# Performance work log

Hardware: AMD Instinct MI355X
Metric: run time of the kernel (lower is better)

## Reference

```python
import jax, jax.numpy as jnp
import numpy as np

N, IN_DIM, HID, OUT, NH = 512, 256, 256, 256, 4
HD = OUT // NH  # head_dim = 64
EPS = 1e-5


def _mlp(x, w1, b1, w2, b2):
    return jax.nn.relu(x @ w1 + b1) @ w2 + b2


def setup_inputs() -> dict:
    key = jax.random.key(0)
    ks = jax.random.split(key, 32)

    def rn(k, shape, fan_in):
        return (jax.random.normal(k, shape, jnp.float32) / np.float32(np.sqrt(fan_in)))

    V = jax.random.normal(ks[0], (N, IN_DIM), jnp.float32)
    adj = jax.random.randint(ks[1], (N, N), 0, 2, jnp.int32)
    adj = adj.at[jnp.arange(N), jnp.arange(N)].set(1)  # self-edges: avoid all -inf rows
    prev_hidden = jax.random.normal(ks[2], (N, HID), jnp.float32)
    z = jnp.zeros
    return dict(
        V=V, adj=adj, prev_hidden=prev_hidden,
        W1=rn(ks[3], (IN_DIM, HID), IN_DIM),
        a_std0=rn(ks[4], (HID, 1), HID), a_std1=rn(ks[5], (HID, 1), HID),
        ce_w1=rn(ks[6], (2 * IN_DIM, HID), 2 * IN_DIM), ce_b1=z((HID,), jnp.float32),
        ce_w2=rn(ks[7], (HID, HD), HID), ce_b2=z((HD,), jnp.float32),
        a_c0=rn(ks[8], (HD, 1), HD), a_c1=rn(ks[9], (HD, 1), HD),
        te_w1=rn(ks[10], (IN_DIM + HID, HID), IN_DIM + HID), te_b1=z((HID,), jnp.float32),
        te_w2=rn(ks[11], (HID, HD), HID), te_b2=z((HD,), jnp.float32),
        a_t0=rn(ks[12], (HD, 1), HD), a_t1=rn(ks[13], (HD, 1), HD),
        co_w1=rn(ks[14], (3 * IN_DIM, HID), 3 * IN_DIM), co_b1=z((HID,), jnp.float32),
        co_w2=rn(ks[15], (HID, HD), HID), co_b2=z((HD,), jnp.float32),
        a_co0=rn(ks[16], (HD, 1), HD), a_co1=rn(ks[17], (HD, 1), HD),
        W2=rn(ks[18], (HID + 2 * HD + 1, OUT), HID + 2 * HD + 1),
        Wo=rn(ks[19], (OUT, OUT), OUT), bo=z((OUT,), jnp.float32),
        ln_g=jnp.ones((OUT,), jnp.float32), ln_b=z((OUT,), jnp.float32),
    )


def reference(V, adj, prev_hidden, W1, a_std0, a_std1,
              ce_w1, ce_b1, ce_w2, ce_b2, a_c0, a_c1,
              te_w1, te_b1, te_w2, te_b2, a_t0, a_t1,
              co_w1, co_b1, co_w2, co_b2, a_co0, a_co1,
              W2, Wo, bo, ln_g, ln_b):
    ninf = -jnp.inf

    # ---- standard GAT branch -> H1: (N, HID) ----
    Wh1 = V @ W1
    s1 = Wh1 @ a_std0 + (Wh1 @ a_std1).T                      # (N, N)
    s1 = jnp.where(adj == 0, ninf, s1)
    H1 = jax.nn.softmax(s1, axis=1) @ Wh1

    # ---- causal branch: all ordered pairs i!=j, global softmax -> H2: (N, HD) ----
    pair = jnp.concatenate([jnp.broadcast_to(V[:, None, :], (N, N, IN_DIM)),
                            jnp.broadcast_to(V[None, :, :], (N, N, IN_DIM))], axis=-1)
    cf = _mlp(pair, ce_w1, ce_b1, ce_w2, ce_b2)               # (N, N, HD)
    cs = (cf @ (a_c0 + a_c1))[..., 0]                         # (N, N)
    cs = jnp.where(jnp.eye(N, dtype=bool), ninf, cs)          # exclude i==j pairs
    ca = jax.nn.softmax(cs.reshape(-1)).reshape(N, N, 1)
    H2 = jnp.broadcast_to((ca * cf).sum((0, 1)), (N, HD))

    # ---- temporal branch: (N,1) scores broadcast against causal mask -> running mean ----
    tf = _mlp(jnp.concatenate([V, prev_hidden], axis=-1), te_w1, te_b1, te_w2, te_b2)  # (N, HD)
    ts = tf @ (a_t0 + a_t1)                                   # (N, 1)
    cmask = jnp.triu(jnp.ones((N, N), bool), 1)
    tsb = jnp.where(cmask, ninf, jnp.broadcast_to(ts, (N, N)))
    H3 = jax.nn.softmax(tsb, axis=1) @ tf                     # (N, HD)

    # ---- coop branch: first two neighbors by index; size-1 softmax; buggy pad -> (N,1) ----
    order = jnp.argsort((1 - adj).astype(jnp.int32), axis=1, stable=True)  # adj==1 first, index order
    nb = V[order[:, :2]]                                      # (N, 2, IN_DIM)
    valid = ((adj == 1).sum(axis=1) >= 2)
    nb = jnp.where(valid[:, None, None], nb, jnp.zeros_like(nb))
    ci = jnp.concatenate([V, nb[:, 0], nb[:, 1]], axis=-1)    # (N, 3*IN_DIM)
    cf4 = _mlp(ci, co_w1, co_b1, co_w2, co_b2)                # (N, HD)
    ca4 = jax.nn.softmax(cf4 @ (a_co0 + a_co1), axis=1)       # (N,1): softmax over size-1 -> ones
    h4vec = (ca4.T @ cf4)[0]                                  # (HD,)
    # original: squeeze(-2)->(HD,), dim==1 -> unsqueeze(-1)->(HD,1), zero-pad rows to N
    H4 = jnp.zeros((N, 1), V.dtype).at[:HD, 0].set(h4vec)

    # ---- combine, lazy W2, proj, LN, ELU (dropout identity in eval) ----
    Hc = jnp.concatenate([H1, H2, H3, H4], axis=-1) @ W2      # (N, OUT)
    out = Hc @ Wo + bo
    mu = out.mean(-1, keepdims=True)
    var = ((out - mu) ** 2).mean(-1, keepdims=True)
    out = (out - mu) / jnp.sqrt(var + EPS) * ln_g + ln_b
    return jax.nn.elu(out)
```

## Files before the change

### kernel.cpp

```cpp
#include <hip/hip_runtime.h>
#include <math.h>

#define NN 512
#define HD 64
#define EPSV 1e-5f

struct GD {
  const float *A, *A2, *A3, *A4;
  const int* I;
  const float *B, *bias;
  float* C;
  int M, K, Nn, mode, act;
};

#define GEMM_SMEM (8704 + 17408 + 2176)
#define MEGA_SMEM 38656

__device__ __forceinline__ void gemm_body(char* smem, const GD& d, int bx, int by) {
  float (*At)[34] = (float (*)[34])smem;
  float (*Bs)[68] = (float (*)[68])(smem + 8704);
  char* extra = smem + 8704 + 17408;
  int* nbl = (int*)extra;
  float* wscl = (float*)extra;
  float* rowsuml = wscl + 512;

  const int t = threadIdx.x;
  const int tx = t & 15, ty = t >> 4;
  const int rowbase = by * 32, colbase = bx * 64;
  const int K = d.K, Nn = d.Nn, mode = d.mode, M = d.M;
  if (rowbase >= M) return;

  if (mode == 2) {
    int wave = t >> 6, lane = t & 63;
    for (int rr = wave; rr < 32; rr += 4) {
      int row = rowbase + rr;
      int n0 = -1, n1 = -1, cnt = 0;
      for (int c = 0; c < 8; ++c) {
        unsigned long long mm = __ballot(d.I[row * NN + c * 64 + lane] != 0);
        cnt += (int)__popcll(mm);
        if (n0 < 0 && mm) { n0 = c * 64 + (int)__builtin_ctzll(mm); mm &= mm - 1; }
        if (n1 < 0 && mm) { n1 = c * 64 + (int)__builtin_ctzll(mm); }
      }
      if (lane == 0) { nbl[rr * 3] = n0; nbl[rr * 3 + 1] = n1; nbl[rr * 3 + 2] = (cnt >= 2); }
    }
    __syncthreads();
  } else if (mode == 4) {
    wscl[t] = d.A2[t];
    wscl[256 + t] = d.A2[256 + t];
    __syncthreads();
  }

  float4 aR[2], bR[4];
  float rs0 = 0.f, rs1 = 0.f;

  auto loadA = [&](int k0) {
#pragma unroll
    for (int j = 0; j < 2; ++j) {
      int idx = t + j * 256;
      int r = idx >> 4, c0 = (idx & 15) * 4;
      int row = rowbase + r, gk = k0 + c0;
      float4 v4 = make_float4(0.f, 0.f, 0.f, 0.f);
      if (mode == 0) {
        if (row < M && gk < K) v4 = *(const float4*)&d.A[(size_t)row * K + gk];
      } else if (mode == 1) {
        if (gk < 256) v4 = *(const float4*)&d.A[row * 256 + gk];
        else v4 = *(const float4*)&d.A2[row * 256 + gk - 256];
      } else if (mode == 2) {
        int seg = gk >> 8;
        int src = (seg == 0) ? row : (nbl[r * 3 + 2] ? nbl[r * 3 + seg - 1] : -1);
        if (src >= 0) v4 = *(const float4*)&d.A[src * 256 + (gk & 255)];
      } else if (mode == 3) {
        if (gk + 3 < 256) v4 = *(const float4*)&d.A[row * 256 + gk];
        else if (gk >= 256 && gk + 3 < 320) v4 = *(const float4*)&d.A2[gk - 256];
        else if (gk >= 320 && gk + 3 < 384) v4 = *(const float4*)&d.A3[row * 64 + gk - 320];
        else if (gk == 384) v4.x = (row < 64) ? d.A4[row] : 0.f;
      } else {
        int4 a4 = *(const int4*)&d.I[row * NN + gk];
        v4.x = a4.x ? wscl[gk + 0] : 0.f;
        v4.y = a4.y ? wscl[gk + 1] : 0.f;
        v4.z = a4.z ? wscl[gk + 2] : 0.f;
        v4.w = a4.w ? wscl[gk + 3] : 0.f;
        float ss = v4.x + v4.y + v4.z + v4.w;
        if (j == 0) rs0 += ss; else rs1 += ss;
      }
      aR[j] = v4;
    }
  };
  auto loadB = [&](int k0) {
#pragma unroll
    for (int j = 0; j < 4; ++j) {
      int idx = t + j * 256;
      int r = idx >> 4, c0 = (idx & 15) * 4;
      int gk = k0 + r;
      float4 v4 = make_float4(0.f, 0.f, 0.f, 0.f);
      if (gk < K) v4 = *(const float4*)&d.B[(size_t)gk * Nn + colbase + c0];
      bR[j] = v4;
    }
  };
  auto stos = [&]() {
#pragma unroll
    for (int j = 0; j < 2; ++j) {
      int idx = t + j * 256;
      int r = idx >> 4, c0 = (idx & 15) * 4;
      At[c0 + 0][r] = aR[j].x;
      At[c0 + 1][r] = aR[j].y;
      At[c0 + 2][r] = aR[j].z;
      At[c0 + 3][r] = aR[j].w;
    }
#pragma unroll
    for (int j = 0; j < 4; ++j) {
      int idx = t + j * 256;
      int r = idx >> 4, c0 = (idx & 15) * 4;
      *(float4*)&Bs[r][c0] = bR[j];
    }
  };

  float4 acc0 = make_float4(0.f, 0.f, 0.f, 0.f);
  float4 acc1 = make_float4(0.f, 0.f, 0.f, 0.f);

  int iters = (K + 63) >> 6;
  loadA(0); loadB(0);
  for (int it = 0; it < iters; ++it) {
    stos();
    __syncthreads();
    if (it + 1 < iters) { loadA((it + 1) << 6); loadB((it + 1) << 6); }
#pragma unroll 8
    for (int kk = 0; kk < 64; ++kk) {
      float2 a = *(const float2*)&At[kk][ty * 2];
      float4 b = *(const float4*)&Bs[kk][tx * 4];
      acc0.x += a.x * b.x; acc0.y += a.x * b.y; acc0.z += a.x * b.z; acc0.w += a.x * b.w;
      acc1.x += a.y * b.x; acc1.y += a.y * b.y; acc1.z += a.y * b.z; acc1.w += a.y * b.w;
    }
    __syncthreads();
  }

  if (mode == 4) {
    float a0 = rs0, a1 = rs1;
#pragma unroll
    for (int off = 8; off; off >>= 1) {
      a0 += __shfl_xor(a0, off, 16);
      a1 += __shfl_xor(a1, off, 16);
    }
    if ((t & 15) == 0) { rowsuml[t >> 4] = a0; rowsuml[16 + (t >> 4)] = a1; }
    __syncthreads();
  }

  int col = colbase + tx * 4;
  float4 bv = make_float4(0.f, 0.f, 0.f, 0.f);
  if (d.bias) bv = *(const float4*)&d.bias[col];
  int row0 = rowbase + ty * 2;
  float4 o0, o1;
  o0.x = acc0.x + bv.x; o0.y = acc0.y + bv.y; o0.z = acc0.z + bv.z; o0.w = acc0.w + bv.w;
  o1.x = acc1.x + bv.x; o1.y = acc1.y + bv.y; o1.z = acc1.z + bv.z; o1.w = acc1.w + bv.w;
  if (d.act) {
    o0.x = fmaxf(o0.x, 0.f); o0.y = fmaxf(o0.y, 0.f); o0.z = fmaxf(o0.z, 0.f); o0.w = fmaxf(o0.w, 0.f);
    o1.x = fmaxf(o1.x, 0.f); o1.y = fmaxf(o1.y, 0.f); o1.z = fmaxf(o1.z, 0.f); o1.w = fmaxf(o1.w, 0.f);
  }
  if (mode == 4) {
    float s0 = 1.f / rowsuml[ty * 2], s1 = 1.f / rowsuml[ty * 2 + 1];
    o0.x *= s0; o0.y *= s0; o0.z *= s0; o0.w *= s0;
    o1.x *= s1; o1.y *= s1; o1.z *= s1; o1.w *= s1;
  }
  if (row0 < M)     *(float4*)&d.C[(size_t)row0 * Nn + col] = o0;
  if (row0 + 1 < M) *(float4*)&d.C[(size_t)(row0 + 1) * Nn + col] = o1;
}

__device__ void wsc_body(char* smem, const GD& d, int grp) {
  const float* W1 = d.A;
  const float* a_std1 = d.A2;
  const float* V = d.A3;
  float* expwsc = d.C;
  float* asl = (float*)smem;
  float* ul  = asl + 256;
  int t = threadIdx.x;
  asl[t] = a_std1[t];
  __syncthreads();
  {
    float s = 0.f;
    const float* wr = W1 + t * 256;
    for (int h = 0; h < 256; h += 4) {
      float4 w4 = *(const float4*)&wr[h];
      float4 a4 = *(const float4*)&asl[h];
      s += w4.x * a4.x + w4.y * a4.y + w4.z * a4.z + w4.w * a4.w;
    }
    ul[t] = s;
  }
  __syncthreads();
  int wave = t >> 6, lane = t & 63;
  float4 u4 = *(const float4*)&ul[lane * 4];
  int j0 = grp * 128;
  for (int j = j0 + wave; j < j0 + 128; j += 4) {
    float4 v4 = *(const float4*)&V[j * 256 + lane * 4];
    float s = v4.x * u4.x + v4.y * u4.y + v4.z * u4.z + v4.w * u4.w;
#pragma unroll
    for (int off = 32; off; off >>= 1) s += __shfl_xor(s, off, 64);
    if (lane == 0) expwsc[j] = __expf(s);
  }
}

struct GD7 { GD d[7]; };
__global__ __launch_bounds__(256) void gemm7_k(GD7 ds) {
  __shared__ __align__(16) char smem[GEMM_SMEM];
  int z = blockIdx.z;
  if (z == 6) {
    if (blockIdx.y != 0) return;
    wsc_body(smem, ds.d[6], blockIdx.x);
    return;
  }
  gemm_body(smem, ds.d[z], blockIdx.x, blockIdx.y);
}
__global__ __launch_bounds__(256) void gemm1_k(GD d) {
  __shared__ __align__(16) char smem[GEMM_SMEM];
  gemm_body(smem, d, blockIdx.x, blockIdx.y);
}

struct MegaArgs {
  const float *P, *Q, *b1, *ce_w2, *a_c0, *a_c1;
  float *mpart, *dpart, *spart;
  GD gH1, gTf, gCf;
};

__device__ void pair_body(char* smem, const MegaArgs& pa, int byy, int bxx) {
  float* Pl  = (float*)smem;
  float* Ql  = Pl + 16 * 260;
  float* el  = Ql + 16 * 260;
  float* wcl = el + 16 * 20;
  float* red = wcl + 256;
  float* sk  = red + 256;
  float* sbl = sk + 256;
  int t = threadIdx.x;

  if (t < 64) red[t] = pa.a_c0[t] + pa.a_c1[t];
  __syncthreads();
  {
    float s = 0.f;
    const float* w2r = pa.ce_w2 + t * 64;
#pragma unroll 8
    for (int h = 0; h < 64; ++h) s += w2r[h] * red[h];
    wcl[t] = s;
  }
  int i0 = byy * 16, j0 = bxx * 16;
  for (int e = t; e < 1024; e += 256) {
    int r = e >> 6, c4 = (e & 63) * 4;
    float4 bb = *(const float4*)&pa.b1[c4];
    float4 pv = *(const float4*)&pa.P[(i0 + r) * 256 + c4];
    pv.x += bb.x; pv.y += bb.y; pv.z += bb.z; pv.w += bb.w;
    *(float4*)&Pl[r * 260 + c4] = pv;
    *(float4*)&Ql[r * 260 + c4] = *(const float4*)&pa.Q[(j0 + r) * 256 + c4];
  }
  __syncthreads();

  int a = t >> 4, b = t & 15;
  const float* pr = &Pl[a * 260];
  const float* qr = &Ql[b * 260];
  float4 c4a = make_float4(0.f, 0.f, 0.f, 0.f);
#pragma unroll 8
  for (int k4 = 0; k4 < 64; ++k4) {
    float4 w = *(const float4*)&wcl[k4 * 4];
    float4 p = *(const float4*)&pr[k4 * 4];
    float4 q = *(const float4*)&qr[k4 * 4];
    c4a.x += fmaxf(p.x + q.x, 0.f) * w.x;
    c4a.y += fmaxf(p.y + q.y, 0.f) * w.y;
    c4a.z += fmaxf(p.z + q.z, 0.f) * w.z;
    c4a.w += fmaxf(p.w + q.w, 0.f) * w.w;
  }
  float s = c4a.x + c4a.y + c4a.z + c4a.w;
  if (i0 + a == j0 + b) s = -INFINITY;
  red[t] = s; __syncthreads();
  for (int ss = 128; ss; ss >>= 1) { if (t < ss) red[t] = fmaxf(red[t], red[t + ss]); __syncthreads(); }
  float mb = red[0];
  __syncthreads();
  float e = __expf(s - mb);
  el[a * 20 + b] = e;
  red[t] = e; __syncthreads();
  for (int ss = 128; ss; ss >>= 1) { if (t < ss) red[t] += red[t + ss]; __syncthreads(); }
  float db = red[0];
  __syncthreads();

  float qv[16];
#pragma unroll
  for (int j = 0; j < 16; ++j) qv[j] = Ql[j * 260 + t];
  float rk = 0.f;
#pragma unroll 4
  for (int i = 0; i < 16; ++i) {
    float pv = Pl[i * 260 + t];
    const float* erow = &el[i * 20];
#pragma unroll
    for (int j4 = 0; j4 < 4; ++j4) {
      float4 e4 = *(const float4*)&erow[j4 * 4];
      rk += e4.x * fmaxf(pv + qv[j4 * 4 + 0], 0.f);
      rk += e4.y * fmaxf(pv + qv[j4 * 4 + 1], 0.f);
      rk += e4.z * fmaxf(pv + qv[j4 * 4 + 2], 0.f);
      rk += e4.w * fmaxf(pv + qv[j4 * 4 + 3], 0.f);
    }
  }
  sk[t] = rk;
  __syncthreads();
  {
    int h = t & 63, q = t >> 6;
    float s2 = 0.f;
    for (int k = q * 64; k < q * 64 + 64; ++k) s2 += sk[k] * pa.ce_w2[k * 64 + h];
    sbl[q * 64 + h] = s2;
  }
  __syncthreads();
  int blk = byy * 32 + bxx;
  if (t < 64) pa.spart[blk * 64 + t] = sbl[t] + sbl[64 + t] + sbl[128 + t] + sbl[192 + t];
  if (t == 0) { pa.mpart[blk] = mb; pa.dpart[blk] = db; }
}

__global__ __launch_bounds__(256) void mega_k(MegaArgs a) {
  __shared__ __align__(16) char smem[MEGA_SMEM];
  int b = blockIdx.x;
  if (b < 64) {
    gemm_body(smem, a.gH1, b & 3, b >> 2);
  } else if (b < 80) {
    gemm_body(smem, a.gTf, 0, b - 64);
  } else if (b < 96) {
    gemm_body(smem, a.gCf, 0, b - 80);
  } else {
    int p = b - 96;
    pair_body(smem, a, p >> 5, p & 31);
  }
}

__global__ __launch_bounds__(1024) void mini_k(
    const float* __restrict__ mpart, const float* __restrict__ dpart,
    const float* __restrict__ spart, const float* __restrict__ ce_b2,
    float* __restrict__ H2row,
    const float* __restrict__ tf, float* __restrict__ H3,
    const float* __restrict__ cf4, float* __restrict__ h4vec) {
  __shared__ float A[1024];
  __shared__ float Bsh[1024];
  __shared__ float segsum[16][65];
  int b = blockIdx.x, t = threadIdx.x;
  if (b == 0) {
    float mv = mpart[t];
    A[t] = mv; __syncthreads();
    for (int s = 512; s; s >>= 1) { if (t < s) A[t] = fmaxf(A[t], A[t + s]); __syncthreads(); }
    float M = A[0];
    __syncthreads();
    float e = __expf(mv - M);
    Bsh[t] = e;
    A[t] = e * dpart[t];
    __syncthreads();
    for (int s = 512; s; s >>= 1) { if (t < s) A[t] += A[t + s]; __syncthreads(); }
    float D = A[0];
    __syncthreads();
    int h = t & 63, g = t >> 6;
    float s2 = 0.f;
    for (int b2 = g * 64; b2 < g * 64 + 64; ++b2) s2 += Bsh[b2] * spart[b2 * 64 + h];
    A[t] = s2;
    __syncthreads();
    for (int p = 8; p; p >>= 1) { if (g < p) A[g * 64 + h] += A[(g + p) * 64 + h]; __syncthreads(); }
    if (t < 64) H2row[t] = A[t] / D + ce_b2[t];
  } else if (b == 1) {
    int h = t & 63, g = t >> 6;
    float vals[32];
    float run = 0.f;
#pragma unroll
    for (int r = 0; r < 32; ++r) { run += tf[(g * 32 + r) * 64 + h]; vals[r] = run; }
    segsum[g][h] = run;
    __syncthreads();
    float off = 0.f;
    for (int gg = 0; gg < g; ++gg) off += segsum[gg][h];
#pragma unroll
    for (int r = 0; r < 32; ++r) {
      int i = g * 32 + r;
      H3[i * 64 + h] = (vals[r] + off) / (float)(i + 1);
    }
  } else {
    int h = t & 63, g = t >> 6;
    float s = 0.f;
    for (int r = 0; r < 32; ++r) s += cf4[(g * 32 + r) * 64 + h];
    A[g * 64 + h] = s;
    __syncthreads();
    for (int p = 8; p; p >>= 1) { if (g < p) A[g * 64 + h] += A[(g + p) * 64 + h]; __syncthreads(); }
    if (t < 64) h4vec[t] = A[t];
  }
}

__global__ void ln_elu_kernel(const float* __restrict__ X, const float* __restrict__ g,
                              const float* __restrict__ b, float* __restrict__ out) {
  __shared__ float red[256];
  int i = blockIdx.x, tid = threadIdx.x;
  float x = X[i * 256 + tid];
  red[tid] = x; __syncthreads();
  for (int s = 128; s; s >>= 1) { if (tid < s) red[tid] += red[tid + s]; __syncthreads(); }
  float mu = red[0] * (1.f / 256.f);
  __syncthreads();
  float d = x - mu;
  red[tid] = d * d; __syncthreads();
  for (int s = 128; s; s >>= 1) { if (tid < s) red[tid] += red[tid + s]; __syncthreads(); }
  float var = red[0] * (1.f / 256.f);
  float y = d / sqrtf(var + EPSV) * g[tid] + b[tid];
  out[i * 256 + tid] = (y > 0.f) ? y : (expf(y) - 1.f);
}

static GD mkgd(const float* A, const float* A2, const float* A3, const float* A4,
               const int* I, const float* B, const float* bias, float* C,
               int M, int K, int Nn, int mode, int act) {
  GD g{A, A2, A3, A4, I, B, bias, C, M, K, Nn, mode, act};
  return g;
}

extern "C" void kernel_launch(void* const* d_in, const int* in_sizes, int n_in,
                              void* d_out, int out_size, void* d_ws, size_t ws_size,
                              hipStream_t stream) {
  const float* V      = (const float*)d_in[0];
  const int*   adj    = (const int*)  d_in[1];
  const float* ph     = (const float*)d_in[2];
  const float* W1     = (const float*)d_in[3];
  const float* a_std1 = (const float*)d_in[5];
  const float* ce_w1  = (const float*)d_in[6];
  const float* ce_b1  = (const float*)d_in[7];
  const float* ce_w2  = (const float*)d_in[8];
  const float* ce_b2  = (const float*)d_in[9];
  const float* a_c0   = (const float*)d_in[10];
  const float* a_c1   = (const float*)d_in[11];
  const float* te_w1  = (const float*)d_in[12];
  const float* te_b1  = (const float*)d_in[13];
  const float* te_w2  = (const float*)d_in[14];
  const float* te_b2  = (const float*)d_in[15];
  const float* co_w1  = (const float*)d_in[18];
  const float* co_b1  = (const float*)d_in[19];
  const float* co_w2  = (const float*)d_in[20];
  const float* co_b2  = (const float*)d_in[21];
  const float* W2     = (const float*)d_in[24];
  const float* Wo     = (const float*)d_in[25];
  const float* bo     = (const float*)d_in[26];
  const float* ln_g   = (const float*)d_in[27];
  const float* ln_b   = (const float*)d_in[28];
  float* out = (float*)d_out;

  float* ws = (float*)d_ws;
  size_t off = 0;
  auto alloc = [&](size_t n) { float* p = ws + off; off += (n + 15) & ~(size_t)15; return p; };

  float* Wh1    = alloc(512 * 256);
  float* Pb     = alloc(512 * 256);
  float* Qb     = alloc(512 * 256);
  float* tfh    = alloc(512 * 256);
  float* cf4h   = alloc(512 * 256);
  float* H1     = alloc(512 * 256);
  float* Wfused = alloc(385 * 256);
  float* T2     = alloc(512 * 256);
  float* tf     = alloc(512 * 64);
  float* cf4    = alloc(512 * 64);
  float* H3     = alloc(512 * 64);
  float* spart  = alloc(1024 * 64);
  float* mpart  = alloc(1024);
  float* dpart  = alloc(1024);
  float* expwsc = alloc(512);
  float* H2row  = alloc(64);
  float* h4vec  = alloc(64);
  (void)ws_size; (void)in_sizes; (void)n_in; (void)out_size;

  GD7 sA;
  sA.d[0] = mkgd(V, 0, 0, 0, 0, W1, 0, Wh1, 512, 256, 256, 0, 0);
  sA.d[1] = mkgd(V, 0, 0, 0, 0, ce_w1, 0, Pb, 512, 256, 256, 0, 0);
  sA.d[2] = mkgd(V, 0, 0, 0, 0, ce_w1 + 256 * 256, 0, Qb, 512, 256, 256, 0, 0);
  sA.d[3] = mkgd(V, ph, 0, 0, 0, te_w1, te_b1, tfh, 512, 512, 256, 1, 1);
  sA.d[4] = mkgd(V, 0, 0, 0, adj, co_w1, co_b1, cf4h, 512, 768, 256, 2, 1);
  sA.d[5] = mkgd(W2, 0, 0, 0, 0, Wo, 0, Wfused, 385, 256, 256, 0, 0);
  sA.d[6] = mkgd(W1, a_std1, V, 0, 0, 0, 0, expwsc, 512, 256, 1, 6, 0);
  gemm7_k<<<dim3(4, 16, 7), 256, 0, stream>>>(sA);

  MegaArgs ma;
  ma.P = Pb; ma.Q = Qb; ma.b1 = ce_b1; ma.ce_w2 = ce_w2;
  ma.a_c0 = a_c0; ma.a_c1 = a_c1;
  ma.mpart = mpart; ma.dpart = dpart; ma.spart = spart;
  ma.gH1 = mkgd(0, expwsc, 0, 0, adj, Wh1, 0, H1, 512, 512, 256, 4, 0);
  ma.gTf = mkgd(tfh, 0, 0, 0, 0, te_w2, te_b2, tf, 512, 256, 64, 0, 0);
  ma.gCf = mkgd(cf4h, 0, 0, 0, 0, co_w2, co_b2, cf4, 512, 256, 64, 0, 0);
  mega_k<<<1120, 256, 0, stream>>>(ma);

  mini_k<<<3, 1024, 0, stream>>>(mpart, dpart, spart, ce_b2, H2row, tf, H3, cf4, h4vec);

  GD gF = mkgd(H1, H2row, H3, h4vec, 0, Wfused, bo, T2, 512, 385, 256, 3, 0);
  gemm1_k<<<dim3(4, 16), 256, 0, stream>>>(gF);

  ln_elu_kernel<<<512, 256, 0, stream>>>(T2, ln_g, ln_b, out);
}
```

Baseline: 204.2 us.

## Pass pair/wsc args as restrict pointers, shrink mini_k block, reorder GEMM z-slices

pair_body and wsc_body now take raw __restrict__ pointers instead of struct references, which may let the compiler hoist and cache loads. mini_k drops from 1024 to 256 threads per block, with each thread covering four times as many rows in its reductions and prefix scan. The z-slices of the first batched GEMM launch are reordered so the heavier K=768 and K=512 GEMMs dispatch first. Fewer threads in mini_k means longer serial loops per thread, trading parallelism for fewer barriers.

```diff
diff --git a/kernel.cpp b/kernel.cpp
--- a/kernel.cpp
+++ b/kernel.cpp
@@ -165,11 +165,8 @@
   if (row0 + 1 < M) *(float4*)&d.C[(size_t)(row0 + 1) * Nn + col] = o1;
 }
 
-__device__ void wsc_body(char* smem, const GD& d, int grp) {
-  const float* W1 = d.A;
-  const float* a_std1 = d.A2;
-  const float* V = d.A3;
-  float* expwsc = d.C;
+__device__ void wsc_body(char* smem, const float* W1, const float* a_std1,
+                         const float* V, float* expwsc, int grp) {
   float* asl = (float*)smem;
   float* ul  = asl + 256;
   int t = threadIdx.x;
@@ -204,7 +201,7 @@
   int z = blockIdx.z;
   if (z == 6) {
     if (blockIdx.y != 0) return;
-    wsc_body(smem, ds.d[6], blockIdx.x);
+    wsc_body(smem, ds.d[6].A, ds.d[6].A2, ds.d[6].A3, ds.d[6].C, blockIdx.x);
     return;
   }
   gemm_body(smem, ds.d[z], blockIdx.x, blockIdx.y);
@@ -214,13 +211,12 @@
   gemm_body(smem, d, blockIdx.x, blockIdx.y);
 }
 
-struct MegaArgs {
-  const float *P, *Q, *b1, *ce_w2, *a_c0, *a_c1;
-  float *mpart, *dpart, *spart;
-  GD gH1, gTf, gCf;
-};
-
-__device__ void pair_body(char* smem, const MegaArgs& pa, int byy, int bxx) {
+__device__ void pair_body(char* smem,
+    const float* __restrict__ P, const float* __restrict__ Q,
+    const float* __restrict__ b1, const float* __restrict__ ce_w2,
+    const float* __restrict__ a_c0, const float* __restrict__ a_c1,
+    float* __restrict__ mpart, float* __restrict__ dpart,
+    float* __restrict__ spart, int byy, int bxx) {
   float* Pl  = (float*)smem;
   float* Ql  = Pl + 16 * 260;
   float* el  = Ql + 16 * 260;
@@ -230,11 +226,11 @@
   float* sbl = sk + 256;
   int t = threadIdx.x;
 
-  if (t < 64) red[t] = pa.a_c0[t] + pa.a_c1[t];
+  if (t < 64) red[t] = a_c0[t] + a_c1[t];
   __syncthreads();
   {
     float s = 0.f;
-    const float* w2r = pa.ce_w2 + t * 64;
+    const float* w2r = ce_w2 + t * 64;
 #pragma unroll 8
     for (int h = 0; h < 64; ++h) s += w2r[h] * red[h];
     wcl[t] = s;
@@ -242,11 +238,11 @@
   int i0 = byy * 16, j0 = bxx * 16;
   for (int e = t; e < 1024; e += 256) {
     int r = e >> 6, c4 = (e & 63) * 4;
-    float4 bb = *(const float4*)&pa.b1[c4];
-    float4 pv = *(const float4*)&pa.P[(i0 + r) * 256 + c4];
+    float4 bb = *(const float4*)&b1[c4];
+    float4 pv = *(const float4*)&P[(i0 + r) * 256 + c4];
     pv.x += bb.x; pv.y += bb.y; pv.z += bb.z; pv.w += bb.w;
     *(float4*)&Pl[r * 260 + c4] = pv;
-    *(float4*)&Ql[r * 260 + c4] = *(const float4*)&pa.Q[(j0 + r) * 256 + c4];
+    *(float4*)&Ql[r * 260 + c4] = *(const float4*)&Q[(j0 + r) * 256 + c4];
   }
   __syncthreads();
 
@@ -299,14 +295,20 @@
   {
     int h = t & 63, q = t >> 6;
     float s2 = 0.f;
-    for (int k = q * 64; k < q * 64 + 64; ++k) s2 += sk[k] * pa.ce_w2[k * 64 + h];
+    for (int k = q * 64; k < q * 64 + 64; ++k) s2 += sk[k] * ce_w2[k * 64 + h];
     sbl[q * 64 + h] = s2;
   }
   __syncthreads();
   int blk = byy * 32 + bxx;
-  if (t < 64) pa.spart[blk * 64 + t] = sbl[t] + sbl[64 + t] + sbl[128 + t] + sbl[192 + t];
-  if (t == 0) { pa.mpart[blk] = mb; pa.dpart[blk] = db; }
-}
+  if (t < 64) spart[blk * 64 + t] = sbl[t] + sbl[64 + t] + sbl[128 + t] + sbl[192 + t];
+  if (t == 0) { mpart[blk] = mb; dpart[blk] = db; }
+}
+
+struct MegaArgs {
+  const float *P, *Q, *b1, *ce_w2, *a_c0, *a_c1;
+  float *mpart, *dpart, *spart;
+  GD gH1, gTf, gCf;
+};
 
 __global__ __launch_bounds__(256) void mega_k(MegaArgs a) {
   __shared__ __align__(16) char smem[MEGA_SMEM];
@@ -319,63 +321,64 @@
     gemm_body(smem, a.gCf, 0, b - 80);
   } else {
     int p = b - 96;
-    pair_body(smem, a, p >> 5, p & 31);
-  }
-}
-
-__global__ __launch_bounds__(1024) void mini_k(
+    pair_body(smem, a.P, a.Q, a.b1, a.ce_w2, a.a_c0, a.a_c1,
+              a.mpart, a.dpart, a.spart, p >> 5, p & 31);
+  }
+}
+
+__global__ __launch_bounds__(256) void mini_k(
     const float* __restrict__ mpart, const float* __restrict__ dpart,
     const float* __restrict__ spart, const float* __restrict__ ce_b2,
     float* __restrict__ H2row,
     const float* __restrict__ tf, float* __restrict__ H3,
     const float* __restrict__ cf4, float* __restrict__ h4vec) {
-  __shared__ float A[1024];
-  __shared__ float Bsh[1024];
-  __shared__ float segsum[16][65];
+  __shared__ float eb[1024];
+  __shared__ float red[256];
   int b = blockIdx.x, t = threadIdx.x;
   if (b == 0) {
-    float mv = mpart[t];
-    A[t] = mv; __syncthreads();
-    for (int s = 512; s; s >>= 1) { if (t < s) A[t] = fmaxf(A[t], A[t + s]); __syncthreads(); }
-    float M = A[0];
-    __syncthreads();
-    float e = __expf(mv - M);
-    Bsh[t] = e;
-    A[t] = e * dpart[t];
-    __syncthreads();
-    for (int s = 512; s; s >>= 1) { if (t < s) A[t] += A[t + s]; __syncthreads(); }
-    float D = A[0];
-    __syncthreads();
+    float m = -INFINITY;
+#pragma unroll
+    for (int c = 0; c < 4; ++c) m = fmaxf(m, mpart[c * 256 + t]);
+    red[t] = m; __syncthreads();
+    for (int s = 128; s; s >>= 1) { if (t < s) red[t] = fmaxf(red[t], red[t + s]); __syncthreads(); }
+    float M = red[0]; __syncthreads();
+    float dsum = 0.f;
+#pragma unroll
+    for (int c = 0; c < 4; ++c) {
+      float e = __expf(mpart[c * 256 + t] - M);
+      eb[c * 256 + t] = e;
+      dsum += e * dpart[c * 256 + t];
+    }
+    red[t] = dsum; __syncthreads();
+    for (int s = 128; s; s >>= 1) { if (t < s) red[t] += red[t + s]; __syncthreads(); }
+    float D = red[0]; __syncthreads();
     int h = t & 63, g = t >> 6;
     float s2 = 0.f;
-    for (int b2 = g * 64; b2 < g * 64 + 64; ++b2) s2 += Bsh[b2] * spart[b2 * 64 + h];
-    A[t] = s2;
-    __syncthreads();
-    for (int p = 8; p; p >>= 1) { if (g < p) A[g * 64 + h] += A[(g + p) * 64 + h]; __syncthreads(); }
-    if (t < 64) H2row[t] = A[t] / D + ce_b2[t];
+    for (int b2 = g * 256; b2 < g * 256 + 256; ++b2) s2 += eb[b2] * spart[b2 * 64 + h];
+    red[t] = s2; __syncthreads();
+    for (int p = 2; p; p >>= 1) { if (g < p) red[g * 64 + h] += red[(g + p) * 64 + h]; __syncthreads(); }
+    if (t < 64) H2row[t] = red[t] / D + ce_b2[t];
   } else if (b == 1) {
     int h = t & 63, g = t >> 6;
-    float vals[32];
     float run = 0.f;
-#pragma unroll
-    for (int r = 0; r < 32; ++r) { run += tf[(g * 32 + r) * 64 + h]; vals[r] = run; }
-    segsum[g][h] = run;
+    for (int r = 0; r < 128; ++r) run += tf[((g << 7) + r) * 64 + h];
+    eb[g * 64 + h] = run;
     __syncthreads();
     float off = 0.f;
-    for (int gg = 0; gg < g; ++gg) off += segsum[gg][h];
-#pragma unroll
-    for (int r = 0; r < 32; ++r) {
-      int i = g * 32 + r;
-      H3[i * 64 + h] = (vals[r] + off) / (float)(i + 1);
+    for (int gg = 0; gg < g; ++gg) off += eb[gg * 64 + h];
+    run = off;
+    for (int r = 0; r < 128; ++r) {
+      int i = (g << 7) + r;
+      run += tf[i * 64 + h];
+      H3[i * 64 + h] = run / (float)(i + 1);
     }
   } else {
     int h = t & 63, g = t >> 6;
     float s = 0.f;
-    for (int r = 0; r < 32; ++r) s += cf4[(g * 32 + r) * 64 + h];
-    A[g * 64 + h] = s;
-    __syncthreads();
-    for (int p = 8; p; p >>= 1) { if (g < p) A[g * 64 + h] += A[(g + p) * 64 + h]; __syncthreads(); }
-    if (t < 64) h4vec[t] = A[t];
+    for (int r = 0; r < 128; ++r) s += cf4[((g << 7) + r) * 64 + h];
+    red[t] = s; __syncthreads();
+    for (int p = 2; p; p >>= 1) { if (g < p) red[g * 64 + h] += red[(g + p) * 64 + h]; __syncthreads(); }
+    if (t < 64) h4vec[t] = red[t];
   }
 }
 
@@ -456,11 +459,11 @@
   (void)ws_size; (void)in_sizes; (void)n_in; (void)out_size;
 
   GD7 sA;
-  sA.d[0] = mkgd(V, 0, 0, 0, 0, W1, 0, Wh1, 512, 256, 256, 0, 0);
-  sA.d[1] = mkgd(V, 0, 0, 0, 0, ce_w1, 0, Pb, 512, 256, 256, 0, 0);
-  sA.d[2] = mkgd(V, 0, 0, 0, 0, ce_w1 + 256 * 256, 0, Qb, 512, 256, 256, 0, 0);
-  sA.d[3] = mkgd(V, ph, 0, 0, 0, te_w1, te_b1, tfh, 512, 512, 256, 1, 1);
-  sA.d[4] = mkgd(V, 0, 0, 0, adj, co_w1, co_b1, cf4h, 512, 768, 256, 2, 1);
+  sA.d[0] = mkgd(V, 0, 0, 0, adj, co_w1, co_b1, cf4h, 512, 768, 256, 2, 1);
+  sA.d[1] = mkgd(V, ph, 0, 0, 0, te_w1, te_b1, tfh, 512, 512, 256, 1, 1);
+  sA.d[2] = mkgd(V, 0, 0, 0, 0, W1, 0, Wh1, 512, 256, 256, 0, 0);
+  sA.d[3] = mkgd(V, 0, 0, 0, 0, ce_w1, 0, Pb, 512, 256, 256, 0, 0);
+  sA.d[4] = mkgd(V, 0, 0, 0, 0, ce_w1 + 256 * 256, 0, Qb, 512, 256, 256, 0, 0);
   sA.d[5] = mkgd(W2, 0, 0, 0, 0, Wo, 0, Wfused, 385, 256, 256, 0, 0);
   sA.d[6] = mkgd(W1, a_std1, V, 0, 0, 0, 0, expwsc, 512, 256, 1, 6, 0);
   gemm7_k<<<dim3(4, 16, 7), 256, 0, stream>>>(sA);
@@ -474,7 +477,7 @@
   ma.gCf = mkgd(cf4h, 0, 0, 0, 0, co_w2, co_b2, cf4, 512, 256, 64, 0, 0);
   mega_k<<<1120, 256, 0, stream>>>(ma);
 
-  mini_k<<<3, 1024, 0, stream>>>(mpart, dpart, spart, ce_b2, H2row, tf, H3, cf4, h4vec);
+  mini_k<<<3, 256, 0, stream>>>(mpart, dpart, spart, ce_b2, H2row, tf, H3, cf4, h4vec);
 
   GD gF = mkgd(H1, H2row, H3, h4vec, 0, Wfused, bo, T2, 512, 385, 256, 3, 0);
   gemm1_k<<<dim3(4, 16), 256, 0, stream>>>(gF);
```

Measured after the change: 210.2 us. +2.9%, slower.
